# Performance work log

Measured on AMD Instinct MI355X. Metric: run time of the kernel, lower is better.

## Reference

```python
import jax, jax.numpy as jnp
import numpy as np

NOISE_STD = 0.01  # noise_std init arg


def setup_inputs() -> dict:
    key = jax.random.key(0)
    k1, k2, k3, k4, k5 = jax.random.split(key, 5)
    B, C, H, W = 32, 256, 56, 56
    x = jax.random.normal(k1, (B, C, H, W), dtype=jnp.float32)
    H_real = jax.random.normal(k2, (B, C, C), dtype=jnp.float32)
    H_imag = jax.random.normal(k3, (B, C, C), dtype=jnp.float32)
    noise_real = jax.random.normal(k4, (B, C, H, W), dtype=jnp.float32)
    noise_imag = jax.random.normal(k5, (B, C, H, W), dtype=jnp.float32)
    return {"x": x, "H_real": H_real, "H_imag": H_imag,
            "noise_real": noise_real, "noise_imag": noise_imag}


def reference(x, H_real, H_imag, noise_real, noise_imag):
    # x: (B,C,H,W) real. Per-batch complex MIMO channel Hc = (Hr + i*Hi)/sqrt(2*C).
    # Since x has zero imaginary part, y = Hc @ x splits into two real GEMMs.
    C = x.shape[1]
    scale = 1.0 / jnp.sqrt(jnp.asarray(2.0 * C, dtype=x.dtype))
    yr = jnp.einsum('bij,bjhw->bihw', H_real, x) * scale + noise_real * NOISE_STD
    yi = jnp.einsum('bij,bjhw->bihw', H_imag, x) * scale + noise_imag * NOISE_STD
    # output_mode == 'magnitude' -> |y|
    return jnp.sqrt(yr * yr + yi * yi)
```

## Files before the change

### kernel.cpp

```cpp
#include <hip/hip_runtime.h>
#include <hip/hip_bf16.h>
#include <math.h>


#define NBATCH 32
#define NC 256
#define NP 3136
#define BM 128
#define BN 64
#define BK 32
#define NBN 49
#define NKI 8

typedef __attribute__((ext_vector_type(8))) short short8;
typedef __attribute__((ext_vector_type(4))) float f32x4;

static __device__ __forceinline__ void gload16(const void* g, void* l) {
  __builtin_amdgcn_global_load_lds(
      (const __attribute__((address_space(1))) void*)g,
      (__attribute__((address_space(3))) void*)l, 16, 0, 0);
}

static __device__ __forceinline__ unsigned short bfr(float f) {
  __hip_bfloat16 h = __float2bfloat16(f);
  return *reinterpret_cast<unsigned short*>(&h);
}

__global__ __launch_bounds__(256)
void perm_h_kernel(const float* __restrict__ hr, const float* __restrict__ hi,
                   unsigned short* __restrict__ ws)
{
  const int blk   = blockIdx.x;
  const int kt    = blk & 7;
  const int b2m   = blk >> 3;
  const int plane = threadIdx.x >> 7;
  const int row   = threadIdx.x & 127;
  const int b     = b2m >> 1;
  const int bm    = b2m & 1;

  const float* src = (plane ? hi : hr)
      + ((size_t)b * NC + bm * 128 + row) * NC + kt * 32;
  unsigned short* dst = ws + ((size_t)(b2m * 8 + kt) * 2 + plane) * 4096 + row * 8;

  #pragma unroll
  for (int fq = 0; fq < 4; ++fq) {
    const float4 v0 = *reinterpret_cast<const float4*>(src + fq * 8);
    const float4 v1 = *reinterpret_cast<const float4*>(src + fq * 8 + 4);
    union { uint4 v; unsigned short u[8]; } o;
    o.u[0] = bfr(v0.x); o.u[1] = bfr(v0.y); o.u[2] = bfr(v0.z); o.u[3] = bfr(v0.w);
    o.u[4] = bfr(v1.x); o.u[5] = bfr(v1.y); o.u[6] = bfr(v1.z); o.u[7] = bfr(v1.w);
    *reinterpret_cast<uint4*>(dst + fq * 1024) = o.v;
  }
}

template<int PRE>
__global__ __launch_bounds__(512, 4)
void rayleigh_main(const float* __restrict__ xg,
                   const float* __restrict__ Hrg,
                   const float* __restrict__ Hig,
                   const unsigned short* __restrict__ Hperm,
                   const float* __restrict__ nrg,
                   const float* __restrict__ nig,
                   float* __restrict__ outg)
{
  __shared__ float x_lds[2][BK * BN];
  __shared__ unsigned short hr_lds[2][4096];
  __shared__ unsigned short hi_lds[2][4096];

  const int raw = blockIdx.x;
  const int v   = (raw & 7) * 392 + (raw >> 3);
  const int b   = v / 98;
  const int r2  = v - b * 98;
  const int bm  = r2 / 49;
  const int bn  = r2 - bm * 49;

  const int tid  = threadIdx.x;
  const int lane = tid & 63;
  const int wave = tid >> 6;
  const int wm   = wave >> 2;
  const int wn   = wave & 3;
  const int fr   = lane & 15;
  const int fq   = lane >> 4;

  const float* xsrc = xg + (size_t)b * NC * NP + (size_t)bn * BN;
  const size_t hrowbase = (size_t)b * NC + bm * BM;
  const size_t hpbase   = (size_t)((b * 2 + bm) * 8);

  auto stage = [&](int t, int buf) {
    {
      const int C16 = wave * 64 + lane;
      const int k   = C16 >> 4;
      const int cp  = C16 & 15;
      const int fqk = k >> 3;
      const int cl  = cp ^ (((fqk & 1) << 2) | (fqk >> 1));
      const float* src = xsrc + (size_t)(t * BK + k) * NP + cl * 4;
      gload16(src, (char*)x_lds[buf] + wave * 1024);
    }
    if constexpr (PRE) {
      #pragma unroll
      for (int i = 0; i < 2; ++i) {
        const int c     = wave * 2 + i;
        const int plane = c >> 3;
        const int fqc   = (c >> 1) & 3;
        const int half  = c & 1;
        unsigned short* hl = plane ? hi_lds[buf] : hr_lds[buf];
        const unsigned short* src = Hperm
            + ((hpbase + t) * 2 + plane) * 4096
            + fqc * 1024 + (half * 64 + lane) * 8;
        gload16(src, (char*)hl + fqc * 2048 + half * 1024);
      }
    }
  };

  f32x4 accR[4], accI[4];
  #pragma unroll
  for (int m = 0; m < 4; ++m) {
    accR[m] = (f32x4){0.f, 0.f, 0.f, 0.f};
    accI[m] = (f32x4){0.f, 0.f, 0.f, 0.f};
  }
  float nrv[4][4], niv[4][4];

  const size_t obase = ((size_t)b * NC + bm * BM + wm * 64 + fq * 4) * NP
                     + (size_t)bn * BN + wn * 16 + fr;
  const int xork = ((fq & 1) << 6) | ((fq >> 1) << 4);
  const int pcol = ((wn * 16 + fr) << 2) ^ xork;

  stage(0, 0);

  #pragma unroll
  for (int t = 0; t < NKI; ++t) {
    if constexpr (PRE) {
      if (t == 0) asm volatile("s_waitcnt vmcnt(0)" ::: "memory");
      else        asm volatile("s_waitcnt vmcnt(4)" ::: "memory");
      __builtin_amdgcn_s_barrier();
      __builtin_amdgcn_sched_barrier(0);
    } else {
      __syncthreads();
    }
    if (t + 1 < NKI) stage(t + 1, (t + 1) & 1);

    {
      const int m = t >> 1, rb = (t & 1) * 2;
      #pragma unroll
      for (int r = 0; r < 2; ++r) {
        const size_t idx = obase + (size_t)(m * 16 + rb + r) * NP;
        nrv[m][rb + r] = __builtin_nontemporal_load(nrg + idx);
        niv[m][rb + r] = __builtin_nontemporal_load(nig + idx);
      }
    }

    const char* xbuf = (const char*)x_lds[t & 1];
    union { short8 s; unsigned short u[8]; } u;
    #pragma unroll
    for (int j = 0; j < 8; ++j) {
      const float f = *reinterpret_cast<const float*>(xbuf + ((fq * 8 + j) << 8) + pcol);
      u.u[j] = bfr(f);
    }
    const short8 xb = u.s;

    #pragma unroll
    for (int m = 0; m < 4; ++m) {
      const int row = wm * 64 + m * 16 + fr;
      short8 ar, ai;
      if constexpr (PRE) {
        ar = *reinterpret_cast<const short8*>(&hr_lds[t & 1][fq * 1024 + row * 8]);
        ai = *reinterpret_cast<const short8*>(&hi_lds[t & 1][fq * 1024 + row * 8]);
      } else {
        const float* p1 = Hrg + (hrowbase + row) * NC + t * 32 + fq * 8;
        const float* p2 = Hig + (hrowbase + row) * NC + t * 32 + fq * 8;
        const float4 v0 = *reinterpret_cast<const float4*>(p1);
        const float4 v1 = *reinterpret_cast<const float4*>(p1 + 4);
        const float4 w0 = *reinterpret_cast<const float4*>(p2);
        const float4 w1 = *reinterpret_cast<const float4*>(p2 + 4);
        union { short8 s; unsigned short uu[8]; } a1, a2;
        a1.uu[0] = bfr(v0.x); a1.uu[1] = bfr(v0.y); a1.uu[2] = bfr(v0.z); a1.uu[3] = bfr(v0.w);
        a1.uu[4] = bfr(v1.x); a1.uu[5] = bfr(v1.y); a1.uu[6] = bfr(v1.z); a1.uu[7] = bfr(v1.w);
        a2.uu[0] = bfr(w0.x); a2.uu[1] = bfr(w0.y); a2.uu[2] = bfr(w0.z); a2.uu[3] = bfr(w0.w);
        a2.uu[4] = bfr(w1.x); a2.uu[5] = bfr(w1.y); a2.uu[6] = bfr(w1.z); a2.uu[7] = bfr(w1.w);
        ar = a1.s; ai = a2.s;
      }
      accR[m] = __builtin_amdgcn_mfma_f32_16x16x32_bf16(ar, xb, accR[m], 0, 0, 0);
      accI[m] = __builtin_amdgcn_mfma_f32_16x16x32_bf16(ai, xb, accI[m], 0, 0, 0);
    }
  }

  const float scale = 0.04419417382415922f;
  const float nstd  = 0.01f;
  #pragma unroll
  for (int m = 0; m < 4; ++m)
    #pragma unroll
    for (int r = 0; r < 4; ++r) {
      const size_t idx = obase + (size_t)(m * 16 + r) * NP;
      const float yr = accR[m][r] * scale + nrv[m][r] * nstd;
      const float yi = accI[m][r] * scale + niv[m][r] * nstd;
      outg[idx] = sqrtf(yr * yr + yi * yi);
    }
}

extern "C" void kernel_launch(void* const* d_in, const int* in_sizes, int n_in,
                              void* d_out, int out_size, void* d_ws, size_t ws_size,
                              hipStream_t stream) {
  const float* x  = (const float*)d_in[0];
  const float* Hr = (const float*)d_in[1];
  const float* Hi = (const float*)d_in[2];
  const float* nr = (const float*)d_in[3];
  const float* ni = (const float*)d_in[4];
  float* out = (float*)d_out;

  const size_t HN = (size_t)NBATCH * NC * NC;

  if (ws_size >= HN * 2 * sizeof(unsigned short)) {
    unsigned short* hperm = (unsigned short*)d_ws;
    hipLaunchKernelGGL(perm_h_kernel, dim3(512), dim3(256), 0, stream, Hr, Hi, hperm);
    hipLaunchKernelGGL((rayleigh_main<1>), dim3(NBATCH * 2 * NBN), dim3(512), 0, stream,
                       x, Hr, Hi, hperm, nr, ni, out);
  } else {
    hipLaunchKernelGGL((rayleigh_main<0>), dim3(NBATCH * 2 * NBN), dim3(512), 0, stream,
                       x, Hr, Hi, (const unsigned short*)nullptr, nr, ni, out);
  }
}
```

Before: 103.9 us.

## Convert main GEMM kernel to persistent grid with atomic tile counter

Replaces the one-block-per-tile launch with a persistent kernel of 768 blocks that fetch tile indices from a global atomic counter, zeroed by a memset before each launch. Occupancy hint is raised from 4 to 6 blocks per CU. The aim is to cut block launch and tail overhead and to balance load across CUs. In exchange it adds an atomic plus two barriers per tile and an extra memset, and it drops the XCD-aware tile remapping so the L2 locality of x and H across blocks changes.

```diff
diff --git a/kernel.cpp b/kernel.cpp
--- a/kernel.cpp
+++ b/kernel.cpp
@@ -11,6 +11,8 @@
 #define BK 32
 #define NBN 49
 #define NKI 8
+#define NTILES (NBATCH * 2 * NBN)
+#define PGRID 768
 
 typedef __attribute__((ext_vector_type(8))) short short8;
 typedef __attribute__((ext_vector_type(4))) float f32x4;
@@ -53,26 +55,18 @@
   }
 }
 
-template<int PRE>
-__global__ __launch_bounds__(512, 4)
-void rayleigh_main(const float* __restrict__ xg,
-                   const float* __restrict__ Hrg,
-                   const float* __restrict__ Hig,
-                   const unsigned short* __restrict__ Hperm,
-                   const float* __restrict__ nrg,
-                   const float* __restrict__ nig,
-                   float* __restrict__ outg)
+__global__ __launch_bounds__(512, 6)
+void rayleigh_persist(const float* __restrict__ xg,
+                      const unsigned short* __restrict__ Hperm,
+                      const float* __restrict__ nrg,
+                      const float* __restrict__ nig,
+                      float* __restrict__ outg,
+                      int* __restrict__ counter)
 {
   __shared__ float x_lds[2][BK * BN];
   __shared__ unsigned short hr_lds[2][4096];
   __shared__ unsigned short hi_lds[2][4096];
-
-  const int raw = blockIdx.x;
-  const int v   = (raw & 7) * 392 + (raw >> 3);
-  const int b   = v / 98;
-  const int r2  = v - b * 98;
-  const int bm  = r2 / 49;
-  const int bn  = r2 - bm * 49;
+  __shared__ int tile_v;
 
   const int tid  = threadIdx.x;
   const int lane = tid & 63;
@@ -81,22 +75,34 @@
   const int wn   = wave & 3;
   const int fr   = lane & 15;
   const int fq   = lane >> 4;
-
-  const float* xsrc = xg + (size_t)b * NC * NP + (size_t)bn * BN;
-  const size_t hrowbase = (size_t)b * NC + bm * BM;
-  const size_t hpbase   = (size_t)((b * 2 + bm) * 8);
-
-  auto stage = [&](int t, int buf) {
-    {
-      const int C16 = wave * 64 + lane;
-      const int k   = C16 >> 4;
-      const int cp  = C16 & 15;
-      const int fqk = k >> 3;
-      const int cl  = cp ^ (((fqk & 1) << 2) | (fqk >> 1));
-      const float* src = xsrc + (size_t)(t * BK + k) * NP + cl * 4;
-      gload16(src, (char*)x_lds[buf] + wave * 1024);
-    }
-    if constexpr (PRE) {
+  const int xork = ((fq & 1) << 6) | ((fq >> 1) << 4);
+  const int pcol = ((wn * 16 + fr) << 2) ^ xork;
+
+  while (true) {
+    __syncthreads();
+    if (tid == 0) tile_v = atomicAdd(counter, 1);
+    __syncthreads();
+    const int v = tile_v;
+    if (v >= NTILES) break;
+
+    const int b   = v / 98;
+    const int r2  = v - b * 98;
+    const int bm  = r2 / 49;
+    const int bn  = r2 - bm * 49;
+
+    const float* xsrc   = xg + (size_t)b * NC * NP + (size_t)bn * BN;
+    const size_t hpbase = (size_t)((b * 2 + bm) * 8);
+
+    auto stage = [&](int t, int buf) {
+      {
+        const int C16 = wave * 64 + lane;
+        const int k   = C16 >> 4;
+        const int cp  = C16 & 15;
+        const int fqk = k >> 3;
+        const int cl  = cp ^ (((fqk & 1) << 2) | (fqk >> 1));
+        const float* src = xsrc + (size_t)(t * BK + k) * NP + cl * 4;
+        gload16(src, (char*)x_lds[buf] + wave * 1024);
+      }
       #pragma unroll
       for (int i = 0; i < 2; ++i) {
         const int c     = wave * 2 + i;
@@ -109,7 +115,107 @@
             + fqc * 1024 + (half * 64 + lane) * 8;
         gload16(src, (char*)hl + fqc * 2048 + half * 1024);
       }
-    }
+    };
+
+    f32x4 accR[4], accI[4];
+    #pragma unroll
+    for (int m = 0; m < 4; ++m) {
+      accR[m] = (f32x4){0.f, 0.f, 0.f, 0.f};
+      accI[m] = (f32x4){0.f, 0.f, 0.f, 0.f};
+    }
+    float nrv[4][4], niv[4][4];
+
+    const size_t obase = ((size_t)b * NC + bm * BM + wm * 64 + fq * 4) * NP
+                       + (size_t)bn * BN + wn * 16 + fr;
+
+    stage(0, 0);
+
+    #pragma unroll
+    for (int t = 0; t < NKI; ++t) {
+      if (t == 0) asm volatile("s_waitcnt vmcnt(0)" ::: "memory");
+      else        asm volatile("s_waitcnt vmcnt(4)" ::: "memory");
+      __builtin_amdgcn_s_barrier();
+      __builtin_amdgcn_sched_barrier(0);
+      if (t + 1 < NKI) stage(t + 1, (t + 1) & 1);
+
+      {
+        const int m = t >> 1, rb = (t & 1) * 2;
+        #pragma unroll
+        for (int r = 0; r < 2; ++r) {
+          const size_t idx = obase + (size_t)(m * 16 + rb + r) * NP;
+          nrv[m][rb + r] = __builtin_nontemporal_load(nrg + idx);
+          niv[m][rb + r] = __builtin_nontemporal_load(nig + idx);
+        }
+      }
+
+      const char* xbuf = (const char*)x_lds[t & 1];
+      union { short8 s; unsigned short u[8]; } u;
+      #pragma unroll
+      for (int j = 0; j < 8; ++j) {
+        const float f = *reinterpret_cast<const float*>(xbuf + ((fq * 8 + j) << 8) + pcol);
+        u.u[j] = bfr(f);
+      }
+      const short8 xb = u.s;
+
+      #pragma unroll
+      for (int m = 0; m < 4; ++m) {
+        const int row = wm * 64 + m * 16 + fr;
+        const short8 ar = *reinterpret_cast<const short8*>(&hr_lds[t & 1][fq * 1024 + row * 8]);
+        const short8 ai = *reinterpret_cast<const short8*>(&hi_lds[t & 1][fq * 1024 + row * 8]);
+        accR[m] = __builtin_amdgcn_mfma_f32_16x16x32_bf16(ar, xb, accR[m], 0, 0, 0);
+        accI[m] = __builtin_amdgcn_mfma_f32_16x16x32_bf16(ai, xb, accI[m], 0, 0, 0);
+      }
+    }
+
+    const float scale = 0.04419417382415922f;
+    const float nstd  = 0.01f;
+    #pragma unroll
+    for (int m = 0; m < 4; ++m)
+      #pragma unroll
+      for (int r = 0; r < 4; ++r) {
+        const size_t idx = obase + (size_t)(m * 16 + r) * NP;
+        const float yr = accR[m][r] * scale + nrv[m][r] * nstd;
+        const float yi = accI[m][r] * scale + niv[m][r] * nstd;
+        outg[idx] = sqrtf(yr * yr + yi * yi);
+      }
+  }
+}
+
+__global__ __launch_bounds__(512, 4)
+void rayleigh_fallback(const float* __restrict__ xg,
+                       const float* __restrict__ Hrg,
+                       const float* __restrict__ Hig,
+                       const float* __restrict__ nrg,
+                       const float* __restrict__ nig,
+                       float* __restrict__ outg)
+{
+  __shared__ float x_lds[2][BK * BN];
+
+  const int raw = blockIdx.x;
+  const int v   = (raw & 7) * 392 + (raw >> 3);
+  const int b   = v / 98;
+  const int r2  = v - b * 98;
+  const int bm  = r2 / 49;
+  const int bn  = r2 - bm * 49;
+
+  const int tid  = threadIdx.x;
+  const int lane = tid & 63;
+  const int wave = tid >> 6;
+  const int wm   = wave >> 2;
+  const int wn   = wave & 3;
+  const int fr   = lane & 15;
+  const int fq   = lane >> 4;
+
+  const float* xsrc = xg + (size_t)b * NC * NP + (size_t)bn * BN;
+  const size_t hrowbase = (size_t)b * NC + bm * BM;
+
+  auto stage = [&](int t, int buf) {
+    const int C16 = wave * 64 + lane;
+    const int k   = C16 >> 4;
+    const int cp  = C16 & 15;
+    const int fqk = k >> 3;
+    const int cl  = cp ^ (((fqk & 1) << 2) | (fqk >> 1));
+    gload16(xsrc + (size_t)(t * BK + k) * NP + cl * 4, (char*)x_lds[buf] + wave * 1024);
   };
 
   f32x4 accR[4], accI[4];
@@ -120,25 +226,15 @@
   }
   float nrv[4][4], niv[4][4];
 
+  const int xork = ((fq & 1) << 6) | ((fq >> 1) << 4);
+  const int pcol = ((wn * 16 + fr) << 2) ^ xork;
   const size_t obase = ((size_t)b * NC + bm * BM + wm * 64 + fq * 4) * NP
                      + (size_t)bn * BN + wn * 16 + fr;
-  const int xork = ((fq & 1) << 6) | ((fq >> 1) << 4);
-  const int pcol = ((wn * 16 + fr) << 2) ^ xork;
 
   stage(0, 0);
-
-  #pragma unroll
   for (int t = 0; t < NKI; ++t) {
-    if constexpr (PRE) {
-      if (t == 0) asm volatile("s_waitcnt vmcnt(0)" ::: "memory");
-      else        asm volatile("s_waitcnt vmcnt(4)" ::: "memory");
-      __builtin_amdgcn_s_barrier();
-      __builtin_amdgcn_sched_barrier(0);
-    } else {
-      __syncthreads();
-    }
+    __syncthreads();
     if (t + 1 < NKI) stage(t + 1, (t + 1) & 1);
-
     {
       const int m = t >> 1, rb = (t & 1) * 2;
       #pragma unroll
@@ -148,7 +244,6 @@
         niv[m][rb + r] = __builtin_nontemporal_load(nig + idx);
       }
     }
-
     const char* xbuf = (const char*)x_lds[t & 1];
     union { short8 s; unsigned short u[8]; } u;
     #pragma unroll
@@ -157,30 +252,22 @@
       u.u[j] = bfr(f);
     }
     const short8 xb = u.s;
-
     #pragma unroll
     for (int m = 0; m < 4; ++m) {
       const int row = wm * 64 + m * 16 + fr;
-      short8 ar, ai;
-      if constexpr (PRE) {
-        ar = *reinterpret_cast<const short8*>(&hr_lds[t & 1][fq * 1024 + row * 8]);
-        ai = *reinterpret_cast<const short8*>(&hi_lds[t & 1][fq * 1024 + row * 8]);
-      } else {
-        const float* p1 = Hrg + (hrowbase + row) * NC + t * 32 + fq * 8;
-        const float* p2 = Hig + (hrowbase + row) * NC + t * 32 + fq * 8;
-        const float4 v0 = *reinterpret_cast<const float4*>(p1);
-        const float4 v1 = *reinterpret_cast<const float4*>(p1 + 4);
-        const float4 w0 = *reinterpret_cast<const float4*>(p2);
-        const float4 w1 = *reinterpret_cast<const float4*>(p2 + 4);
-        union { short8 s; unsigned short uu[8]; } a1, a2;
-        a1.uu[0] = bfr(v0.x); a1.uu[1] = bfr(v0.y); a1.uu[2] = bfr(v0.z); a1.uu[3] = bfr(v0.w);
-        a1.uu[4] = bfr(v1.x); a1.uu[5] = bfr(v1.y); a1.uu[6] = bfr(v1.z); a1.uu[7] = bfr(v1.w);
-        a2.uu[0] = bfr(w0.x); a2.uu[1] = bfr(w0.y); a2.uu[2] = bfr(w0.z); a2.uu[3] = bfr(w0.w);
-        a2.uu[4] = bfr(w1.x); a2.uu[5] = bfr(w1.y); a2.uu[6] = bfr(w1.z); a2.uu[7] = bfr(w1.w);
-        ar = a1.s; ai = a2.s;
-      }
-      accR[m] = __builtin_amdgcn_mfma_f32_16x16x32_bf16(ar, xb, accR[m], 0, 0, 0);
-      accI[m] = __builtin_amdgcn_mfma_f32_16x16x32_bf16(ai, xb, accI[m], 0, 0, 0);
+      const float* p1 = Hrg + (hrowbase + row) * NC + t * 32 + fq * 8;
+      const float* p2 = Hig + (hrowbase + row) * NC + t * 32 + fq * 8;
+      const float4 v0 = *reinterpret_cast<const float4*>(p1);
+      const float4 v1 = *reinterpret_cast<const float4*>(p1 + 4);
+      const float4 w0 = *reinterpret_cast<const float4*>(p2);
+      const float4 w1 = *reinterpret_cast<const float4*>(p2 + 4);
+      union { short8 s; unsigned short uu[8]; } a1, a2;
+      a1.uu[0] = bfr(v0.x); a1.uu[1] = bfr(v0.y); a1.uu[2] = bfr(v0.z); a1.uu[3] = bfr(v0.w);
+      a1.uu[4] = bfr(v1.x); a1.uu[5] = bfr(v1.y); a1.uu[6] = bfr(v1.z); a1.uu[7] = bfr(v1.w);
+      a2.uu[0] = bfr(w0.x); a2.uu[1] = bfr(w0.y); a2.uu[2] = bfr(w0.z); a2.uu[3] = bfr(w0.w);
+      a2.uu[4] = bfr(w1.x); a2.uu[5] = bfr(w1.y); a2.uu[6] = bfr(w1.z); a2.uu[7] = bfr(w1.w);
+      accR[m] = __builtin_amdgcn_mfma_f32_16x16x32_bf16(a1.s, xb, accR[m], 0, 0, 0);
+      accI[m] = __builtin_amdgcn_mfma_f32_16x16x32_bf16(a2.s, xb, accI[m], 0, 0, 0);
     }
   }
 
@@ -207,15 +294,18 @@
   const float* ni = (const float*)d_in[4];
   float* out = (float*)d_out;
 
-  const size_t HN = (size_t)NBATCH * NC * NC;
-
-  if (ws_size >= HN * 2 * sizeof(unsigned short)) {
+  const size_t HN      = (size_t)NBATCH * NC * NC;
+  const size_t HPBYTES = HN * 2 * sizeof(unsigned short);
+
+  if (ws_size >= HPBYTES + sizeof(int)) {
     unsigned short* hperm = (unsigned short*)d_ws;
+    int* counter = (int*)((char*)d_ws + HPBYTES);
+    hipMemsetAsync(counter, 0, sizeof(int), stream);
     hipLaunchKernelGGL(perm_h_kernel, dim3(512), dim3(256), 0, stream, Hr, Hi, hperm);
-    hipLaunchKernelGGL((rayleigh_main<1>), dim3(NBATCH * 2 * NBN), dim3(512), 0, stream,
-                       x, Hr, Hi, hperm, nr, ni, out);
+    hipLaunchKernelGGL(rayleigh_persist, dim3(PGRID), dim3(512), 0, stream,
+                       x, hperm, nr, ni, out, counter);
   } else {
-    hipLaunchKernelGGL((rayleigh_main<0>), dim3(NBATCH * 2 * NBN), dim3(512), 0, stream,
-                       x, Hr, Hi, (const unsigned short*)nullptr, nr, ni, out);
-  }
-}
+    hipLaunchKernelGGL(rayleigh_fallback, dim3(NTILES), dim3(512), 0, stream,
+                       x, Hr, Hi, nr, ni, out);
+  }
+}
```

After: 176.4 us. +69.8%, slower.
